# Performance work log

Measured on AMD Instinct MI355X. Metric: run time of the kernel, lower is better.

## Reference

```python
import jax, jax.numpy as jnp
import numpy as np

N, D_IN, D_HID, D_CODE, K = 131072, 768, 512, 256, 512

def setup_inputs() -> dict:
    key = jax.random.key(0)
    ks = jax.random.split(key, 10)
    s1 = 1.0 / np.sqrt(D_IN); s2 = 1.0 / np.sqrt(D_HID); s3 = 1.0 / np.sqrt(D_CODE)
    return {
        "x": jax.random.normal(ks[0], (N, D_IN), jnp.float32),
        "W1": jax.random.normal(ks[1], (D_IN, D_HID), jnp.float32) * s1,
        "b1": jnp.zeros((D_HID,), jnp.float32),
        "W2": jax.random.normal(ks[2], (D_HID, D_CODE), jnp.float32) * s2,
        "b2": jnp.zeros((D_CODE,), jnp.float32),
        "codebook": jax.random.normal(ks[3], (K, D_CODE), jnp.float32),
        "W3": jax.random.normal(ks[4], (D_CODE, D_HID), jnp.float32) * s3,
        "b3": jnp.zeros((D_HID,), jnp.float32),
        "W4": jax.random.normal(ks[5], (D_HID, D_IN), jnp.float32) * s2,
        "b4": jnp.zeros((D_IN,), jnp.float32),
    }

def reference(x, W1, b1, W2, b2, codebook, W3, b3, W4, b4):
    # encoder: Linear -> ReLU -> Linear
    z = jax.nn.relu(x @ W1 + b1) @ W2 + b2                      # [N, D_CODE]
    # nearest-code search: squared euclidean distances to codebook
    # ||z||^2 - 2 z.c + ||c||^2  (||z||^2 constant per row, drop for argmin)
    dots = z @ codebook.T                                        # [N, K]
    dist = jnp.sum(codebook * codebook, axis=-1)[None, :] - 2.0 * dots
    indices = jnp.argmin(dist, axis=-1)                          # [N] int
    quantized = codebook[indices]                                # gather [N, D_CODE]
    # commitment loss: mse(quantize.detach(), z) * commitment_weight(=1.0)
    commit_loss = jnp.mean((jax.lax.stop_gradient(quantized) - z) ** 2)
    # straight-through estimator
    quantized_st = z + jax.lax.stop_gradient(quantized - z)
    # decoder: Linear -> ReLU -> Linear
    recon = jax.nn.relu(quantized_st @ W3 + b3) @ W4 + b4        # [N, D_IN]
    return recon, indices.astype(jnp.int32), commit_loss
```

## Files before the change

### kernel.cpp

```cpp
#include <hip/hip_runtime.h>
#include <hip/hip_bf16.h>
#include <math.h>

#define N_ROWS 131072
#define DIN    768
#define DHID   512
#define DCODE  256
#define KC     512
#define NFUSE  768
#define TAU    5e-3f

typedef short short8 __attribute__((ext_vector_type(8)));
typedef float f32x4  __attribute__((ext_vector_type(4)));
typedef unsigned int   u32;
typedef unsigned short u16;

__device__ __forceinline__ void gload16(const void* g, void* l) {
    __builtin_amdgcn_global_load_lds(
        (const __attribute__((address_space(1))) u32*)g,
        (__attribute__((address_space(3))) u32*)l, 16, 0, 0);
}

__device__ __forceinline__ u16 f2bf(float f) {
    u32 u = __builtin_bit_cast(u32, f);
    return (u16)((u + 0x7fffu + ((u >> 16) & 1u)) >> 16);
}
__device__ __forceinline__ float bf2f(u16 h) {
    u32 u = ((u32)h) << 16;
    return __builtin_bit_cast(float, u);
}

__device__ __forceinline__ void xcd_swizzle(int& bxs, int& bys) {
    const int GX  = gridDim.x;
    const int nwg = GX * gridDim.y;
    const int lid = blockIdx.y * GX + blockIdx.x;
    const int chunk = nwg >> 3;
    const int nlid  = (lid & 7) * chunk + (lid >> 3);
    bxs = nlid % GX;
    bys = nlid / GX;
}

__device__ __forceinline__ void split_write(char* hidst, char* lodst, float4 v) {
    u16 h0 = f2bf(v.x), h1 = f2bf(v.y), h2 = f2bf(v.z), h3 = f2bf(v.w);
    u16 l0 = f2bf(__fsub_rn(v.x, bf2f(h0)));
    u16 l1 = f2bf(__fsub_rn(v.y, bf2f(h1)));
    u16 l2 = f2bf(__fsub_rn(v.z, bf2f(h2)));
    u16 l3 = f2bf(__fsub_rn(v.w, bf2f(h3)));
    ushort4 hi; hi.x = h0; hi.y = h1; hi.z = h2; hi.w = h3;
    ushort4 lo; lo.x = l0; lo.y = l1; lo.z = l2; lo.w = l3;
    *(ushort4*)hidst = hi;
    *(ushort4*)lodst = lo;
}

template<int EPI>
__global__ __launch_bounds__(256, 3)
void split2_gemm(const float* __restrict__ Af32,
                 const u16* __restrict__ Ahi, const u16* __restrict__ Alo,
                 const u16* __restrict__ Bhi, const u16* __restrict__ Blo,
                 const float* __restrict__ bias,
                 const float* __restrict__ cnorm,
                 u16* __restrict__ Chi, u16* __restrict__ Clo,
                 float* __restrict__ pd1, int* __restrict__ pi1,
                 float* __restrict__ pd2, float* __restrict__ pzn,
                 int M, int N, int K)
{
    __shared__ char lds[32768];
    const int t = threadIdx.x, lane = t & 63, wid = t >> 6;
    const int wm = wid >> 1, wn = wid & 1;
    int bxs, bys; xcd_swizzle(bxs, bys);
    const int bm = bys * 128, bn = bxs * 128;
    const bool full3 = (EPI == 0) || (bxs < 4);

    const int sr = lane >> 3, qq = lane & 7, sl = qq ^ sr;
    const u16* bsrc[4];
    #pragma unroll
    for (int c = 0; c < 4; c++) {
        int row = bn + (wid * 4 + c) * 8 + sr;
        const u16* base = (sl < 4) ? Bhi : Blo;
        bsrc[c] = base + (size_t)row * K + (sl & 3) * 8;
    }
    const u16* asrc[4];
    const float* a32src[4];
    int adhi[4], adlo[4];
    if constexpr (EPI == 1) {
        #pragma unroll
        for (int c = 0; c < 4; c++) {
            int row = bm + (wid * 4 + c) * 8 + sr;
            const u16* base = (sl < 4) ? Ahi : Alo;
            asrc[c] = base + (size_t)row * K + (sl & 3) * 8;
        }
    } else {
        #pragma unroll
        for (int c = 0; c < 4; c++) {
            int id = c * 256 + t;
            int row = id >> 3, k4 = id & 7;
            a32src[c] = Af32 + (size_t)(bm + row) * K + k4 * 4;
            int s = k4 >> 1, hf = k4 & 1;
            adhi[c] = row * 128 + ((s ^ (row & 7)) << 4) + hf * 8;
            adlo[c] = row * 128 + (((s | 4) ^ (row & 7)) << 4) + hf * 8;
        }
    }

    f32x4 acc[4][4];
    #pragma unroll
    for (int i = 0; i < 4; i++)
        #pragma unroll
        for (int j = 0; j < 4; j++) acc[i][j] = (f32x4)0.f;

    const int fr = lane & 15, sw = lane & 7;
    const int offhi = (((lane >> 4) ^ sw) << 4);
    const int offlo = ((((lane >> 4) | 4) ^ sw) << 4);
    const int arow = wm * 64 + fr, brow = wn * 64 + fr;
    const int NT = K >> 5;

    for (int tt = 0; tt < NT; tt++) {
        __syncthreads();
        const int kadv = tt * 32;
        #pragma unroll
        for (int c = 0; c < 4; c++)
            gload16(bsrc[c] + kadv, lds + 16384 + (wid * 4 + c) * 1024);
        if constexpr (EPI == 1) {
            #pragma unroll
            for (int c = 0; c < 4; c++)
                gload16(asrc[c] + kadv, lds + (wid * 4 + c) * 1024);
        } else {
            #pragma unroll
            for (int c = 0; c < 4; c++) {
                float4 v = *(const float4*)(a32src[c] + kadv);
                split_write(lds + adhi[c], lds + adlo[c], v);
            }
        }
        __syncthreads();
        char* ab  = lds;
        char* bb2 = lds + 16384;
        short8 ah[4], al[4];
        #pragma unroll
        for (int i = 0; i < 4; i++) {
            ah[i] = *(const short8*)(ab + ((arow + i * 16) << 7) + offhi);
            al[i] = *(const short8*)(ab + ((arow + i * 16) << 7) + offlo);
        }
        if (full3) {
            #pragma unroll
            for (int j = 0; j < 4; j++) {
                short8 bh = *(const short8*)(bb2 + ((brow + j * 16) << 7) + offhi);
                short8 bl = *(const short8*)(bb2 + ((brow + j * 16) << 7) + offlo);
                #pragma unroll
                for (int i = 0; i < 4; i++) {
                    acc[i][j] = __builtin_amdgcn_mfma_f32_16x16x32_bf16(ah[i], bh, acc[i][j], 0, 0, 0);
                    acc[i][j] = __builtin_amdgcn_mfma_f32_16x16x32_bf16(al[i], bh, acc[i][j], 0, 0, 0);
                    acc[i][j] = __builtin_amdgcn_mfma_f32_16x16x32_bf16(ah[i], bl, acc[i][j], 0, 0, 0);
                }
            }
        } else {
            #pragma unroll
            for (int j = 0; j < 4; j++) {
                short8 bh = *(const short8*)(bb2 + ((brow + j * 16) << 7) + offhi);
                #pragma unroll
                for (int i = 0; i < 4; i++)
                    acc[i][j] = __builtin_amdgcn_mfma_f32_16x16x32_bf16(ah[i], bh, acc[i][j], 0, 0, 0);
            }
        }
    }

    if constexpr (EPI == 1) {
        const int ec = lane & 15, g = lane >> 4;
        if (bxs < 4) {
            float cnv[4], bcv[4];
            #pragma unroll
            for (int j = 0; j < 4; j++) {
                int c = bn + wn * 64 + j * 16 + ec;
                cnv[j] = cnorm[c]; bcv[j] = bias[c];
            }
            const int strip = bxs * 2 + wn;
            #pragma unroll
            for (int i = 0; i < 4; i++) {
                #pragma unroll
                for (int e = 0; e < 4; e++) {
                    float d1 = INFINITY, d2 = INFINITY; int i1 = 0x7fffffff;
                    #pragma unroll
                    for (int j = 0; j < 4; j++) {
                        int c = bn + wn * 64 + j * 16 + ec;
                        float d = __fsub_rn(cnv[j],
                                  __fmul_rn(2.0f, __fadd_rn(acc[i][j][e], bcv[j])));
                        if (d < d1 || (d == d1 && c < i1)) { d2 = d1; d1 = d; i1 = c; }
                        else if (d < d2) d2 = d;
                    }
                    #pragma unroll
                    for (int m = 1; m < 16; m <<= 1) {
                        float od1 = __shfl_xor(d1, m);
                        int   oi1 = __shfl_xor(i1, m);
                        float od2 = __shfl_xor(d2, m);
                        if (od1 < d1 || (od1 == d1 && oi1 < i1)) {
                            d2 = fminf(d1, od2); d1 = od1; i1 = oi1;
                        } else d2 = fminf(d2, od1);
                    }
                    if (ec == 0) {
                        int r = bm + wm * 64 + i * 16 + g * 4 + e;
                        pd1[(size_t)strip * M + r] = d1;
                        pi1[(size_t)strip * M + r] = i1;
                        pd2[(size_t)strip * M + r] = d2;
                    }
                }
            }
        } else {
            float bcv[4];
            #pragma unroll
            for (int j = 0; j < 4; j++)
                bcv[j] = bias[bn + wn * 64 + j * 16 + ec];
            const int zs = (bxs - 4) * 2 + wn;
            #pragma unroll
            for (int i = 0; i < 4; i++) {
                #pragma unroll
                for (int e = 0; e < 4; e++) {
                    float s = 0.f;
                    #pragma unroll
                    for (int j = 0; j < 4; j++) {
                        float zv = acc[i][j][e] + bcv[j];
                        s = fmaf(zv, zv, s);
                    }
                    #pragma unroll
                    for (int m = 1; m < 16; m <<= 1) s += __shfl_xor(s, m);
                    if (ec == 0) {
                        int r = bm + wm * 64 + i * 16 + g * 4 + e;
                        pzn[(size_t)zs * M + r] = s;
                    }
                }
            }
        }
        return;
    } else {
        const int er = (lane >> 4) * 4, ec = lane & 15;
        #pragma unroll
        for (int j = 0; j < 4; j++) {
            int col = bn + wn * 64 + j * 16 + ec;
            float bb = bias[col];
            #pragma unroll
            for (int i = 0; i < 4; i++) {
                #pragma unroll
                for (int e = 0; e < 4; e++) {
                    int r = bm + wm * 64 + i * 16 + er + e;
                    float v = fmaxf(__fadd_rn(acc[i][j][e], bb), 0.f);
                    u16 hi = f2bf(v);
                    u16 lo = f2bf(__fsub_rn(v, bf2f(hi)));
                    Chi[(size_t)r * N + col] = hi;
                    Clo[(size_t)r * N + col] = lo;
                }
            }
        }
    }
}

template<bool RELU, bool OUT_BF16>
__global__ __launch_bounds__(256, 3)
void mfma_gemm(const u16* __restrict__ A, const u16* __restrict__ BT,
               const float* __restrict__ bias,
               void* __restrict__ Cout, int M, int N, int K)
{
    __shared__ char lds[32768];
    const int t    = threadIdx.x;
    const int lane = t & 63, wid = t >> 6;
    const int wm   = wid >> 1, wn = wid & 1;
    int bxs, bys;
    xcd_swizzle(bxs, bys);
    const int bm = bys * 128, bn = bxs * 128;

    const int sr = lane >> 3;
    const int sc = ((lane & 7) ^ sr) * 8;
    const u16* aptr[4];
    const u16* bptr[4];
    #pragma unroll
    for (int c = 0; c < 4; c++) {
        int gc   = wid * 4 + c;
        int arow = bm + 8 * gc + sr;
        aptr[c] = A  + (size_t)arow * K + sc;
        int brow = bn + 8 * gc + sr;
        bptr[c] = BT + (size_t)brow * K + sc;
    }

    f32x4 acc[4][4];
    #pragma unroll
    for (int i = 0; i < 4; i++)
        #pragma unroll
        for (int j = 0; j < 4; j++) acc[i][j] = (f32x4)0.f;

    const int koff0 = (16 * (lane >> 4))      ^ ((lane & 7) << 4);
    const int koff1 = (64 + 16 * (lane >> 4)) ^ ((lane & 7) << 4);
    const int arow_rd = wm * 64 + (lane & 15);
    const int brow_rd = wn * 64 + (lane & 15);

    const int NT = K >> 6;
    for (int tt = 0; tt < NT; tt++) {
        __syncthreads();
        const int k0 = tt << 6;
        #pragma unroll
        for (int c = 0; c < 4; c++) {
            int gc = wid * 4 + c;
            gload16(aptr[c] + k0, lds + gc * 1024);
            gload16(bptr[c] + k0, lds + 16384 + gc * 1024);
        }
        __syncthreads();
        char* ldsA = lds;
        char* ldsB = lds + 16384;
        #pragma unroll
        for (int kk = 0; kk < 2; kk++) {
            const int ko = kk ? koff1 : koff0;
            short8 af[4], bfr[4];
            #pragma unroll
            for (int i = 0; i < 4; i++)
                af[i]  = *(const short8*)(ldsA + (arow_rd + i * 16) * 128 + ko);
            #pragma unroll
            for (int j = 0; j < 4; j++)
                bfr[j] = *(const short8*)(ldsB + (brow_rd + j * 16) * 128 + ko);
            #pragma unroll
            for (int i = 0; i < 4; i++)
                #pragma unroll
                for (int j = 0; j < 4; j++)
                    acc[i][j] = __builtin_amdgcn_mfma_f32_16x16x32_bf16(
                        af[i], bfr[j], acc[i][j], 0, 0, 0);
        }
    }

    const int er = (lane >> 4) * 4;
    const int ec = lane & 15;
    #pragma unroll
    for (int j = 0; j < 4; j++) {
        int col  = bn + wn * 64 + j * 16 + ec;
        float bb = bias[col];
        #pragma unroll
        for (int i = 0; i < 4; i++) {
            #pragma unroll
            for (int e = 0; e < 4; e++) {
                int r   = bm + wm * 64 + i * 16 + er + e;
                float v = acc[i][j][e] + bb;
                if (RELU) v = fmaxf(v, 0.f);
                if (OUT_BF16) ((u16*)Cout)[(size_t)r * N + col]  = f2bf(v);
                else          ((float*)Cout)[(size_t)r * N + col] = v;
            }
        }
    }
}

__global__ __launch_bounds__(256)
void gather_out(const float* __restrict__ R, const int* __restrict__ idxi,
                float* __restrict__ out)
{
    int w    = (blockIdx.x * 256 + threadIdx.x) >> 6;
    int lane = threadIdx.x & 63;
    int nw   = (gridDim.x * 256) >> 6;
    for (int r = w; r < N_ROWS; r += nw) {
        int code = idxi[r];
        const float4* src = (const float4*)(R + (size_t)code * DIN);
        float4* dst = (float4*)(out + (size_t)r * DIN);
        dst[lane]       = src[lane];
        dst[lane + 64]  = src[lane + 64];
        dst[lane + 128] = src[lane + 128];
    }
}

__global__ void transpose_cb_kernel(const float* __restrict__ cb, float* __restrict__ cbT)
{
    int tid = blockIdx.x * 256 + threadIdx.x;
    int k = tid >> 8;
    int d = tid & 255;
    cbT[(size_t)d * KC + k] = cb[(size_t)k * DCODE + d];
}

__global__ void cast_bf16_kernel(const float* __restrict__ in, u16* __restrict__ out, int n)
{
    int i = blockIdx.x * 256 + threadIdx.x;
    if (i < n) out[i] = f2bf(in[i]);
}

__global__ void castT_bf16_kernel(const float* __restrict__ in, u16* __restrict__ out,
                                  int K, int N)
{
    int i = blockIdx.x * 256 + threadIdx.x;
    if (i >= K * N) return;
    int n = i / K, k = i - n * K;
    out[i] = f2bf(in[(size_t)k * N + n]);
}

__global__ void prep_W1T(const float* __restrict__ W1, u16* __restrict__ Thi,
                         u16* __restrict__ Tlo)
{
    int id = blockIdx.x * 256 + threadIdx.x;
    if (id >= DHID * DIN) return;
    int n = id / DIN, k = id - n * DIN;
    float v = W1[(size_t)k * DHID + n];
    u16 hi = f2bf(v);
    Thi[id] = hi;
    Tlo[id] = f2bf(__fsub_rn(v, bf2f(hi)));
}

__global__ void prep_Wc(const float* __restrict__ W2, const float* __restrict__ cb,
                        u16* __restrict__ Thi, u16* __restrict__ Tlo)
{
    int id = blockIdx.x * 256 + threadIdx.x;
    int n = id & 511, h = id >> 9;
    double acc = 0.0;
    for (int tt2 = 0; tt2 < DCODE; tt2++)
        acc += (double)W2[(size_t)h * DCODE + tt2] * (double)cb[(size_t)n * DCODE + tt2];
    float v = (float)acc;
    u16 hi = f2bf(v);
    Thi[(size_t)n * DHID + h] = hi;
    Tlo[(size_t)n * DHID + h] = f2bf(__fsub_rn(v, bf2f(hi)));
}

__global__ void prep_W2T_pair(const float* __restrict__ W2, u16* __restrict__ Thi,
                              u16* __restrict__ Tlo)
{
    int id = blockIdx.x * 256 + threadIdx.x;
    if (id >= DCODE * DHID) return;
    int t2 = id >> 9, h = id & 511;
    float v = W2[(size_t)h * DCODE + t2];
    u16 hi = f2bf(v);
    Thi[(size_t)(KC + t2) * DHID + h] = hi;
    Tlo[(size_t)(KC + t2) * DHID + h] = f2bf(__fsub_rn(v, bf2f(hi)));
}

__global__ void prep_bcf(const float* __restrict__ b2, const float* __restrict__ cb,
                         float* __restrict__ bcf)
{
    int n = blockIdx.x * 256 + threadIdx.x;
    if (n >= NFUSE) return;
    if (n < KC) {
        double acc = 0.0;
        for (int tt2 = 0; tt2 < DCODE; tt2++)
            acc += (double)b2[tt2] * (double)cb[(size_t)n * DCODE + tt2];
        bcf[n] = (float)acc;
    } else {
        bcf[n] = b2[n - KC];
    }
}

__global__ void cnorm_np_kernel(const float* __restrict__ cb, float* __restrict__ cnorm)
{
    int k = blockIdx.x * 64 + threadIdx.x;
    if (k >= KC) return;
    const float* c = cb + (size_t)k * DCODE;
    float bsum[2];
    #pragma unroll
    for (int b = 0; b < 2; b++) {
        const float* a = c + b * 128;
        float r[8];
        #pragma unroll
        for (int j = 0; j < 8; j++) r[j] = __fmul_rn(a[j], a[j]);
        for (int i = 8; i < 128; i += 8)
            #pragma unroll
            for (int j = 0; j < 8; j++)
                r[j] = __fadd_rn(r[j], __fmul_rn(a[i + j], a[i + j]));
        bsum[b] = __fadd_rn(
            __fadd_rn(__fadd_rn(r[0], r[1]), __fadd_rn(r[2], r[3])),
            __fadd_rn(__fadd_rn(r[4], r[5]), __fadd_rn(r[6], r[7])));
    }
    cnorm[k] = __fadd_rn(bsum[0], bsum[1]);
}

__global__ void final_argmin_flag(const float* __restrict__ pd1,
                                  const int* __restrict__ pi1,
                                  const float* __restrict__ pd2,
                                  const float* __restrict__ pzn,
                                  float* __restrict__ idx_f,
                                  int* __restrict__ idx_i,
                                  float* __restrict__ rowloss,
                                  int* __restrict__ cnt,
                                  int* __restrict__ list)
{
    int r = blockIdx.x * 256 + threadIdx.x;
    if (r >= N_ROWS) return;
    float d1 = pd1[r]; int i1 = pi1[r]; float d2 = pd2[r];
    #pragma unroll
    for (int b = 1; b < 8; b++) {
        float od1 = pd1[(size_t)b * N_ROWS + r];
        int   oi1 = pi1[(size_t)b * N_ROWS + r];
        float od2 = pd2[(size_t)b * N_ROWS + r];
        if (od1 < d1 || (od1 == d1 && oi1 < i1)) {
            d2 = fminf(d1, od2); d1 = od1; i1 = oi1;
        } else d2 = fminf(d2, od1);
    }
    float zn = pzn[r] + pzn[(size_t)N_ROWS + r]
             + pzn[(size_t)2 * N_ROWS + r] + pzn[(size_t)3 * N_ROWS + r];
    idx_f[r]   = (float)i1;
    idx_i[r]   = i1;
    rowloss[r] = zn + d1;
    if (d2 - d1 < TAU) {
        int p = atomicAdd(cnt, 1);
        list[p] = r;
    }
}

__global__ __launch_bounds__(512)
void recompute_kernel(const float* __restrict__ x,  const float* __restrict__ W1,
                      const float* __restrict__ b1, const float* __restrict__ W2,
                      const float* __restrict__ b2, const float* __restrict__ cbT,
                      const float* __restrict__ cnorm,
                      const int* __restrict__ cnt,  const int* __restrict__ list,
                      float* __restrict__ idx_f,    int* __restrict__ idx_i)
{
    __shared__ float xs[8][DIN];
    __shared__ float h1s[8][DHID];
    __shared__ float zs[8][DCODE];
    __shared__ float swd[8][8];
    __shared__ int   swi[8][8];
    __shared__ int   rls[8];
    const int t = threadIdx.x;
    const int n = *cnt;

    for (int base = blockIdx.x * 8; base < n; base += gridDim.x * 8) {
        __syncthreads();
        if (t < 8) rls[t] = (base + t < n) ? list[base + t] : -1;
        __syncthreads();
        #pragma unroll
        for (int rr = 0; rr < 8; rr++) {
            int row = rls[rr];
            if (row >= 0)
                for (int i = t; i < DIN; i += 512)
                    xs[rr][i] = x[(size_t)row * DIN + i];
        }
        __syncthreads();
        {
            float acc[8] = {0.f,0.f,0.f,0.f,0.f,0.f,0.f,0.f};
            for (int i = 0; i < DIN; i++) {
                float w = W1[(size_t)i * DHID + t];
                #pragma unroll
                for (int rr = 0; rr < 8; rr++)
                    acc[rr] = fmaf(xs[rr][i], w, acc[rr]);
            }
            float bb = b1[t];
            #pragma unroll
            for (int rr = 0; rr < 8; rr++)
                h1s[rr][t] = fmaxf(__fadd_rn(acc[rr], bb), 0.f);
        }
        __syncthreads();
        {
            int half = t >> 8, t2 = t & 255;
            float acc[4] = {0.f,0.f,0.f,0.f};
            for (int h = 0; h < DHID; h++) {
                float w = W2[(size_t)h * DCODE + t2];
                #pragma unroll
                for (int q2 = 0; q2 < 4; q2++)
                    acc[q2] = fmaf(h1s[half * 4 + q2][h], w, acc[q2]);
            }
            float bb = b2[t2];
            #pragma unroll
            for (int q2 = 0; q2 < 4; q2++)
                zs[half * 4 + q2][t2] = __fadd_rn(acc[q2], bb);
        }
        __syncthreads();
        {
            float acc[8] = {0.f,0.f,0.f,0.f,0.f,0.f,0.f,0.f};
            for (int d = 0; d < DCODE; d++) {
                float c = cbT[(size_t)d * KC + t];
                #pragma unroll
                for (int rr = 0; rr < 8; rr++)
                    acc[rr] = fmaf(zs[rr][d], c, acc[rr]);
            }
            float cn = cnorm[t];
            #pragma unroll
            for (int rr = 0; rr < 8; rr++) {
                float d = __fsub_rn(cn, __fmul_rn(2.0f, acc[rr]));
                int ii = t;
                #pragma unroll
                for (int m = 1; m < 64; m <<= 1) {
                    float od = __shfl_xor(d, m);
                    int   oi = __shfl_xor(ii, m);
                    if (od < d || (od == d && oi < ii)) { d = od; ii = oi; }
                }
                if ((t & 63) == 0) { swd[rr][t >> 6] = d; swi[rr][t >> 6] = ii; }
            }
        }
        __syncthreads();
        if (t < 8) {
            int row = rls[t];
            if (row >= 0) {
                float d = swd[t][0]; int ii = swi[t][0];
                #pragma unroll
                for (int w = 1; w < 8; w++) {
                    float od = swd[t][w]; int oi = swi[t][w];
                    if (od < d || (od == d && oi < ii)) { d = od; ii = oi; }
                }
                idx_i[row] = ii;
                idx_f[row] = (float)ii;
            }
        }
    }
}

__global__ void loss_reduce_kernel(const float* __restrict__ rowloss,
                                   double* __restrict__ acc, int n)
{
    double s = 0.0;
    for (int i = blockIdx.x * blockDim.x + threadIdx.x; i < n; i += gridDim.x * blockDim.x)
        s += (double)rowloss[i];
    for (int off = 32; off; off >>= 1) s += __shfl_xor(s, off);
    __shared__ double red[4];
    int lane = threadIdx.x & 63, wave = threadIdx.x >> 6;
    if (lane == 0) red[wave] = s;
    __syncthreads();
    if (threadIdx.x == 0) {
        double b = red[0] + red[1] + red[2] + red[3];
        atomicAdd(acc, b);
    }
}

__global__ void finalize_kernel(const double* __restrict__ acc, float* __restrict__ out)
{
    out[0] = (float)(acc[0] / ((double)N_ROWS * (double)DCODE));
}

extern "C" void kernel_launch(void* const* d_in, const int* in_sizes, int n_in,
                              void* d_out, int out_size, void* d_ws, size_t ws_size,
                              hipStream_t stream)
{
    const float* x  = (const float*)d_in[0];
    const float* W1 = (const float*)d_in[1];
    const float* b1 = (const float*)d_in[2];
    const float* W2 = (const float*)d_in[3];
    const float* b2 = (const float*)d_in[4];
    const float* cb = (const float*)d_in[5];
    const float* W3 = (const float*)d_in[6];
    const float* b3 = (const float*)d_in[7];
    const float* W4 = (const float*)d_in[8];
    const float* b4 = (const float*)d_in[9];
    float* out = (float*)d_out;
    char*  ws  = (char*)d_ws;

    u16*    h1hi    = (u16*)   (ws);
    u16*    h1lo    = (u16*)   (ws + 134217728);
    float*  pd1     = (float*) (ws + 268435456);
    int*    pi1     = (int*)   (ws + 272629760);
    float*  pd2     = (float*) (ws + 276824064);
    float*  pzn     = (float*) (ws + 281018368);
    float*  rowloss = (float*) (ws + 283115520);
    int*    idxi    = (int*)   (ws + 283639808);
    int*    list    = (int*)   (ws + 284164096);
    int*    rcnt    = (int*)   (ws + 284688384);
    double* lossa   = (double*)(ws + 284688448);
    u16*    W1Thi   = (u16*)   (ws + 284688512);
    u16*    W1Tlo   = (u16*)   (ws + 285474944);
    u16*    WfThi   = (u16*)   (ws + 286261376);
    u16*    WfTlo   = (u16*)   (ws + 287047808);
    u16*    cbB     = (u16*)   (ws + 287834240);
    u16*    W3T     = (u16*)   (ws + 288096384);
    u16*    W4T     = (u16*)   (ws + 288358528);
    float*  bcf     = (float*) (ws + 289144960);
    float*  cnorm   = (float*) (ws + 289148032);
    float*  cbT     = (float*) (ws + 289150080);
    u16*    R1b     = (u16*)   (ws + 289674368);
    float*  Rf      = (float*) (ws + 290198656);

    float* idxf    = out + (size_t)N_ROWS * DIN;
    float* lossout = idxf + N_ROWS;

    hipMemsetAsync(ws + 284688384, 0, 128, stream);

    transpose_cb_kernel<<<512, 256, 0, stream>>>(cb, cbT);
    cnorm_np_kernel<<<8, 64, 0, stream>>>(cb, cnorm);
    cast_bf16_kernel<<<(KC*DCODE)/256, 256, 0, stream>>>(cb, cbB, KC*DCODE);
    castT_bf16_kernel<<<(DCODE*DHID)/256, 256, 0, stream>>>(W3, W3T, DCODE, DHID);
    castT_bf16_kernel<<<(DHID*DIN)/256, 256, 0, stream>>>(W4, W4T, DHID, DIN);
    prep_W1T<<<(DHID*DIN)/256, 256, 0, stream>>>(W1, W1Thi, W1Tlo);
    prep_Wc<<<(KC*DHID)/256, 256, 0, stream>>>(W2, cb, WfThi, WfTlo);
    prep_W2T_pair<<<(DCODE*DHID)/256, 256, 0, stream>>>(W2, WfThi, WfTlo);
    prep_bcf<<<3, 256, 0, stream>>>(b2, cb, bcf);

    mfma_gemm<true,  true ><<<dim3(4, 4), 256, 0, stream>>>(
        cbB, W3T, b3, (void*)R1b, KC, DHID, DCODE);
    mfma_gemm<false, false><<<dim3(6, 4), 256, 0, stream>>>(
        R1b, W4T, b4, (void*)Rf, KC, DIN, DHID);

    split2_gemm<0><<<dim3(DHID/128, N_ROWS/128), 256, 0, stream>>>(
        x, nullptr, nullptr, W1Thi, W1Tlo, b1, nullptr,
        h1hi, h1lo, nullptr, nullptr, nullptr, nullptr, N_ROWS, DHID, DIN);
    split2_gemm<1><<<dim3(NFUSE/128, N_ROWS/128), 256, 0, stream>>>(
        nullptr, h1hi, h1lo, WfThi, WfTlo, bcf, cnorm,
        nullptr, nullptr, pd1, pi1, pd2, pzn, N_ROWS, NFUSE, DHID);

    final_argmin_flag<<<N_ROWS/256, 256, 0, stream>>>(
        pd1, pi1, pd2, pzn, idxf, idxi, rowloss, rcnt, list);
    recompute_kernel<<<2048, 512, 0, stream>>>(
        x, W1, b1, W2, b2, cbT, cnorm, rcnt, list, idxf, idxi);

    gather_out<<<4096, 256, 0, stream>>>(Rf, idxi, out);

    loss_reduce_kernel<<<256, 256, 0, stream>>>(rowloss, lossa, N_ROWS);
    finalize_kernel<<<1, 1, 0, stream>>>(lossa, lossout);
}
```

Baseline: 942.0 us.

## Drop split-bf16 emulation; use plain bf16 GEMMs with wider recompute margin

Replaces the three-MFMA hi/lo split-bf16 emulation of fp32 in the encoder and distance GEMMs with single-pass bf16 GEMMs. The hidden activations are stored only as bf16, and the K-step grows from 32 to 64. This removes about two thirds of the MFMA work and half of the h1 traffic. To compensate for lower precision, the near-tie threshold TAU is raised from 5e-3 to 1.5, so many more rows fall into the exact fp32 recompute path, which could become costly.

```diff
diff --git a/kernel.cpp b/kernel.cpp
--- a/kernel.cpp
+++ b/kernel.cpp
@@ -8,7 +8,7 @@
 #define DCODE  256
 #define KC     512
 #define NFUSE  768
-#define TAU    5e-3f
+#define TAU    1.5f
 
 typedef short short8 __attribute__((ext_vector_type(8)));
 typedef float f32x4  __attribute__((ext_vector_type(4)));
@@ -40,210 +40,230 @@
     bys = nlid / GX;
 }
 
-__device__ __forceinline__ void split_write(char* hidst, char* lodst, float4 v) {
-    u16 h0 = f2bf(v.x), h1 = f2bf(v.y), h2 = f2bf(v.z), h3 = f2bf(v.w);
-    u16 l0 = f2bf(__fsub_rn(v.x, bf2f(h0)));
-    u16 l1 = f2bf(__fsub_rn(v.y, bf2f(h1)));
-    u16 l2 = f2bf(__fsub_rn(v.z, bf2f(h2)));
-    u16 l3 = f2bf(__fsub_rn(v.w, bf2f(h3)));
-    ushort4 hi; hi.x = h0; hi.y = h1; hi.z = h2; hi.w = h3;
-    ushort4 lo; lo.x = l0; lo.y = l1; lo.z = l2; lo.w = l3;
-    *(ushort4*)hidst = hi;
-    *(ushort4*)lodst = lo;
-}
-
-template<int EPI>
 __global__ __launch_bounds__(256, 3)
-void split2_gemm(const float* __restrict__ Af32,
-                 const u16* __restrict__ Ahi, const u16* __restrict__ Alo,
-                 const u16* __restrict__ Bhi, const u16* __restrict__ Blo,
-                 const float* __restrict__ bias,
-                 const float* __restrict__ cnorm,
-                 u16* __restrict__ Chi, u16* __restrict__ Clo,
-                 float* __restrict__ pd1, int* __restrict__ pi1,
-                 float* __restrict__ pd2, float* __restrict__ pzn,
-                 int M, int N, int K)
+void h1_gemm(const float* __restrict__ x, const u16* __restrict__ W1T,
+             const float* __restrict__ b1, u16* __restrict__ h1b,
+             int M, int N, int K)
 {
     __shared__ char lds[32768];
     const int t = threadIdx.x, lane = t & 63, wid = t >> 6;
     const int wm = wid >> 1, wn = wid & 1;
     int bxs, bys; xcd_swizzle(bxs, bys);
     const int bm = bys * 128, bn = bxs * 128;
-    const bool full3 = (EPI == 0) || (bxs < 4);
-
-    const int sr = lane >> 3, qq = lane & 7, sl = qq ^ sr;
-    const u16* bsrc[4];
+
+    const int sr = lane >> 3;
+    const int sc = ((lane & 7) ^ sr) * 8;
+    const u16* bptr[4];
     #pragma unroll
     for (int c = 0; c < 4; c++) {
-        int row = bn + (wid * 4 + c) * 8 + sr;
-        const u16* base = (sl < 4) ? Bhi : Blo;
-        bsrc[c] = base + (size_t)row * K + (sl & 3) * 8;
-    }
-    const u16* asrc[4];
-    const float* a32src[4];
-    int adhi[4], adlo[4];
-    if constexpr (EPI == 1) {
+        int brow = bn + 8 * (wid * 4 + c) + sr;
+        bptr[c] = W1T + (size_t)brow * K + sc;
+    }
+    const float* asrc[4];
+    int albyte[4];
+    #pragma unroll
+    for (int c = 0; c < 4; c++) {
+        int id = c * 256 + t;
+        int row = id >> 3, g = id & 7;
+        asrc[c]   = x + (size_t)(bm + row) * K + g * 8;
+        albyte[c] = row * 128 + ((g ^ (row & 7)) << 4);
+    }
+
+    f32x4 acc[4][4];
+    #pragma unroll
+    for (int i = 0; i < 4; i++)
+        #pragma unroll
+        for (int j = 0; j < 4; j++) acc[i][j] = (f32x4)0.f;
+
+    const int koff0 = (16 * (lane >> 4))      ^ ((lane & 7) << 4);
+    const int koff1 = (64 + 16 * (lane >> 4)) ^ ((lane & 7) << 4);
+    const int arow_rd = wm * 64 + (lane & 15);
+    const int brow_rd = wn * 64 + (lane & 15);
+
+    const int NT = K >> 6;
+    for (int tt = 0; tt < NT; tt++) {
+        __syncthreads();
+        const int k0 = tt << 6;
+        #pragma unroll
+        for (int c = 0; c < 4; c++)
+            gload16(bptr[c] + k0, lds + 16384 + (wid * 4 + c) * 1024);
         #pragma unroll
         for (int c = 0; c < 4; c++) {
-            int row = bm + (wid * 4 + c) * 8 + sr;
-            const u16* base = (sl < 4) ? Ahi : Alo;
-            asrc[c] = base + (size_t)row * K + (sl & 3) * 8;
+            float4 v0 = *(const float4*)(asrc[c] + k0);
+            float4 v1 = *(const float4*)(asrc[c] + k0 + 4);
+            short8 p;
+            p[0] = (short)f2bf(v0.x); p[1] = (short)f2bf(v0.y);
+            p[2] = (short)f2bf(v0.z); p[3] = (short)f2bf(v0.w);
+            p[4] = (short)f2bf(v1.x); p[5] = (short)f2bf(v1.y);
+            p[6] = (short)f2bf(v1.z); p[7] = (short)f2bf(v1.w);
+            *(short8*)(lds + albyte[c]) = p;
+        }
+        __syncthreads();
+        char* ldsA = lds;
+        char* ldsB = lds + 16384;
+        #pragma unroll
+        for (int kk = 0; kk < 2; kk++) {
+            const int ko = kk ? koff1 : koff0;
+            short8 af[4], bfr[4];
+            #pragma unroll
+            for (int i = 0; i < 4; i++)
+                af[i]  = *(const short8*)(ldsA + (arow_rd + i * 16) * 128 + ko);
+            #pragma unroll
+            for (int j = 0; j < 4; j++)
+                bfr[j] = *(const short8*)(ldsB + (brow_rd + j * 16) * 128 + ko);
+            #pragma unroll
+            for (int i = 0; i < 4; i++)
+                #pragma unroll
+                for (int j = 0; j < 4; j++)
+                    acc[i][j] = __builtin_amdgcn_mfma_f32_16x16x32_bf16(
+                        af[i], bfr[j], acc[i][j], 0, 0, 0);
+        }
+    }
+
+    const int er = (lane >> 4) * 4, ec = lane & 15;
+    #pragma unroll
+    for (int j = 0; j < 4; j++) {
+        int col  = bn + wn * 64 + j * 16 + ec;
+        float bb = b1[col];
+        #pragma unroll
+        for (int i = 0; i < 4; i++) {
+            #pragma unroll
+            for (int e = 0; e < 4; e++) {
+                int r   = bm + wm * 64 + i * 16 + er + e;
+                float v = fmaxf(acc[i][j][e] + bb, 0.f);
+                h1b[(size_t)r * N + col] = f2bf(v);
+            }
+        }
+    }
+}
+
+__global__ __launch_bounds__(256, 3)
+void dots_gemm(const u16* __restrict__ A, const u16* __restrict__ BT,
+               const float* __restrict__ bias, const float* __restrict__ cnorm,
+               float* __restrict__ pd1, int* __restrict__ pi1,
+               float* __restrict__ pd2, float* __restrict__ pzn,
+               int M, int N, int K)
+{
+    __shared__ char lds[32768];
+    const int t = threadIdx.x, lane = t & 63, wid = t >> 6;
+    const int wm = wid >> 1, wn = wid & 1;
+    int bxs, bys; xcd_swizzle(bxs, bys);
+    const int bm = bys * 128, bn = bxs * 128;
+
+    const int sr = lane >> 3;
+    const int sc = ((lane & 7) ^ sr) * 8;
+    const u16* aptr[4];
+    const u16* bptr[4];
+    #pragma unroll
+    for (int c = 0; c < 4; c++) {
+        int gc = wid * 4 + c;
+        aptr[c] = A  + (size_t)(bm + 8 * gc + sr) * K + sc;
+        bptr[c] = BT + (size_t)(bn + 8 * gc + sr) * K + sc;
+    }
+
+    f32x4 acc[4][4];
+    #pragma unroll
+    for (int i = 0; i < 4; i++)
+        #pragma unroll
+        for (int j = 0; j < 4; j++) acc[i][j] = (f32x4)0.f;
+
+    const int koff0 = (16 * (lane >> 4))      ^ ((lane & 7) << 4);
+    const int koff1 = (64 + 16 * (lane >> 4)) ^ ((lane & 7) << 4);
+    const int arow_rd = wm * 64 + (lane & 15);
+    const int brow_rd = wn * 64 + (lane & 15);
+
+    const int NT = K >> 6;
+    for (int tt = 0; tt < NT; tt++) {
+        __syncthreads();
+        const int k0 = tt << 6;
+        #pragma unroll
+        for (int c = 0; c < 4; c++) {
+            int gc = wid * 4 + c;
+            gload16(aptr[c] + k0, lds + gc * 1024);
+            gload16(bptr[c] + k0, lds + 16384 + gc * 1024);
+        }
+        __syncthreads();
+        char* ldsA = lds;
+        char* ldsB = lds + 16384;
+        #pragma unroll
+        for (int kk = 0; kk < 2; kk++) {
+            const int ko = kk ? koff1 : koff0;
+            short8 af[4], bfr[4];
+            #pragma unroll
+            for (int i = 0; i < 4; i++)
+                af[i]  = *(const short8*)(ldsA + (arow_rd + i * 16) * 128 + ko);
+            #pragma unroll
+            for (int j = 0; j < 4; j++)
+                bfr[j] = *(const short8*)(ldsB + (brow_rd + j * 16) * 128 + ko);
+            #pragma unroll
+            for (int i = 0; i < 4; i++)
+                #pragma unroll
+                for (int j = 0; j < 4; j++)
+                    acc[i][j] = __builtin_amdgcn_mfma_f32_16x16x32_bf16(
+                        af[i], bfr[j], acc[i][j], 0, 0, 0);
+        }
+    }
+
+    const int ec = lane & 15, g = lane >> 4;
+    if (bxs < 4) {
+        float cnv[4], bcv[4];
+        #pragma unroll
+        for (int j = 0; j < 4; j++) {
+            int c = bn + wn * 64 + j * 16 + ec;
+            cnv[j] = cnorm[c]; bcv[j] = bias[c];
+        }
+        const int strip = bxs * 2 + wn;
+        #pragma unroll
+        for (int i = 0; i < 4; i++) {
+            #pragma unroll
+            for (int e = 0; e < 4; e++) {
+                float d1 = INFINITY, d2 = INFINITY; int i1 = 0x7fffffff;
+                #pragma unroll
+                for (int j = 0; j < 4; j++) {
+                    int c = bn + wn * 64 + j * 16 + ec;
+                    float d = __fsub_rn(cnv[j],
+                              __fmul_rn(2.0f, __fadd_rn(acc[i][j][e], bcv[j])));
+                    if (d < d1 || (d == d1 && c < i1)) { d2 = d1; d1 = d; i1 = c; }
+                    else if (d < d2) d2 = d;
+                }
+                #pragma unroll
+                for (int m = 1; m < 16; m <<= 1) {
+                    float od1 = __shfl_xor(d1, m);
+                    int   oi1 = __shfl_xor(i1, m);
+                    float od2 = __shfl_xor(d2, m);
+                    if (od1 < d1 || (od1 == d1 && oi1 < i1)) {
+                        d2 = fminf(d1, od2); d1 = od1; i1 = oi1;
+                    } else d2 = fminf(d2, od1);
+                }
+                if (ec == 0) {
+                    int r = bm + wm * 64 + i * 16 + g * 4 + e;
+                    pd1[(size_t)strip * M + r] = d1;
+                    pi1[(size_t)strip * M + r] = i1;
+                    pd2[(size_t)strip * M + r] = d2;
+                }
+            }
         }
     } else {
-        #pragma unroll
-        for (int c = 0; c < 4; c++) {
-            int id = c * 256 + t;
-            int row = id >> 3, k4 = id & 7;
-            a32src[c] = Af32 + (size_t)(bm + row) * K + k4 * 4;
-            int s = k4 >> 1, hf = k4 & 1;
-            adhi[c] = row * 128 + ((s ^ (row & 7)) << 4) + hf * 8;
-            adlo[c] = row * 128 + (((s | 4) ^ (row & 7)) << 4) + hf * 8;
-        }
-    }
-
-    f32x4 acc[4][4];
-    #pragma unroll
-    for (int i = 0; i < 4; i++)
-        #pragma unroll
-        for (int j = 0; j < 4; j++) acc[i][j] = (f32x4)0.f;
-
-    const int fr = lane & 15, sw = lane & 7;
-    const int offhi = (((lane >> 4) ^ sw) << 4);
-    const int offlo = ((((lane >> 4) | 4) ^ sw) << 4);
-    const int arow = wm * 64 + fr, brow = wn * 64 + fr;
-    const int NT = K >> 5;
-
-    for (int tt = 0; tt < NT; tt++) {
-        __syncthreads();
-        const int kadv = tt * 32;
-        #pragma unroll
-        for (int c = 0; c < 4; c++)
-            gload16(bsrc[c] + kadv, lds + 16384 + (wid * 4 + c) * 1024);
-        if constexpr (EPI == 1) {
-            #pragma unroll
-            for (int c = 0; c < 4; c++)
-                gload16(asrc[c] + kadv, lds + (wid * 4 + c) * 1024);
-        } else {
-            #pragma unroll
-            for (int c = 0; c < 4; c++) {
-                float4 v = *(const float4*)(a32src[c] + kadv);
-                split_write(lds + adhi[c], lds + adlo[c], v);
-            }
-        }
-        __syncthreads();
-        char* ab  = lds;
-        char* bb2 = lds + 16384;
-        short8 ah[4], al[4];
+        float bcv[4];
+        #pragma unroll
+        for (int j = 0; j < 4; j++)
+            bcv[j] = bias[bn + wn * 64 + j * 16 + ec];
+        const int zs = (bxs - 4) * 2 + wn;
         #pragma unroll
         for (int i = 0; i < 4; i++) {
-            ah[i] = *(const short8*)(ab + ((arow + i * 16) << 7) + offhi);
-            al[i] = *(const short8*)(ab + ((arow + i * 16) << 7) + offlo);
-        }
-        if (full3) {
-            #pragma unroll
-            for (int j = 0; j < 4; j++) {
-                short8 bh = *(const short8*)(bb2 + ((brow + j * 16) << 7) + offhi);
-                short8 bl = *(const short8*)(bb2 + ((brow + j * 16) << 7) + offlo);
-                #pragma unroll
-                for (int i = 0; i < 4; i++) {
-                    acc[i][j] = __builtin_amdgcn_mfma_f32_16x16x32_bf16(ah[i], bh, acc[i][j], 0, 0, 0);
-                    acc[i][j] = __builtin_amdgcn_mfma_f32_16x16x32_bf16(al[i], bh, acc[i][j], 0, 0, 0);
-                    acc[i][j] = __builtin_amdgcn_mfma_f32_16x16x32_bf16(ah[i], bl, acc[i][j], 0, 0, 0);
+            #pragma unroll
+            for (int e = 0; e < 4; e++) {
+                float s = 0.f;
+                #pragma unroll
+                for (int j = 0; j < 4; j++) {
+                    float zv = acc[i][j][e] + bcv[j];
+                    s = fmaf(zv, zv, s);
                 }
-            }
-        } else {
-            #pragma unroll
-            for (int j = 0; j < 4; j++) {
-                short8 bh = *(const short8*)(bb2 + ((brow + j * 16) << 7) + offhi);
-                #pragma unroll
-                for (int i = 0; i < 4; i++)
-                    acc[i][j] = __builtin_amdgcn_mfma_f32_16x16x32_bf16(ah[i], bh, acc[i][j], 0, 0, 0);
-            }
-        }
-    }
-
-    if constexpr (EPI == 1) {
-        const int ec = lane & 15, g = lane >> 4;
-        if (bxs < 4) {
-            float cnv[4], bcv[4];
-            #pragma unroll
-            for (int j = 0; j < 4; j++) {
-                int c = bn + wn * 64 + j * 16 + ec;
-                cnv[j] = cnorm[c]; bcv[j] = bias[c];
-            }
-            const int strip = bxs * 2 + wn;
-            #pragma unroll
-            for (int i = 0; i < 4; i++) {
-                #pragma unroll
-                for (int e = 0; e < 4; e++) {
-                    float d1 = INFINITY, d2 = INFINITY; int i1 = 0x7fffffff;
-                    #pragma unroll
-                    for (int j = 0; j < 4; j++) {
-                        int c = bn + wn * 64 + j * 16 + ec;
-                        float d = __fsub_rn(cnv[j],
-                                  __fmul_rn(2.0f, __fadd_rn(acc[i][j][e], bcv[j])));
-                        if (d < d1 || (d == d1 && c < i1)) { d2 = d1; d1 = d; i1 = c; }
-                        else if (d < d2) d2 = d;
-                    }
-                    #pragma unroll
-                    for (int m = 1; m < 16; m <<= 1) {
-                        float od1 = __shfl_xor(d1, m);
-                        int   oi1 = __shfl_xor(i1, m);
-                        float od2 = __shfl_xor(d2, m);
-                        if (od1 < d1 || (od1 == d1 && oi1 < i1)) {
-                            d2 = fminf(d1, od2); d1 = od1; i1 = oi1;
-                        } else d2 = fminf(d2, od1);
-                    }
-                    if (ec == 0) {
-                        int r = bm + wm * 64 + i * 16 + g * 4 + e;
-                        pd1[(size_t)strip * M + r] = d1;
-                        pi1[(size_t)strip * M + r] = i1;
-                        pd2[(size_t)strip * M + r] = d2;
-                    }
-                }
-            }
-        } else {
-            float bcv[4];
-            #pragma unroll
-            for (int j = 0; j < 4; j++)
-                bcv[j] = bias[bn + wn * 64 + j * 16 + ec];
-            const int zs = (bxs - 4) * 2 + wn;
-            #pragma unroll
-            for (int i = 0; i < 4; i++) {
-                #pragma unroll
-                for (int e = 0; e < 4; e++) {
-                    float s = 0.f;
-                    #pragma unroll
-                    for (int j = 0; j < 4; j++) {
-                        float zv = acc[i][j][e] + bcv[j];
-                        s = fmaf(zv, zv, s);
-                    }
-                    #pragma unroll
-                    for (int m = 1; m < 16; m <<= 1) s += __shfl_xor(s, m);
-                    if (ec == 0) {
-                        int r = bm + wm * 64 + i * 16 + g * 4 + e;
-                        pzn[(size_t)zs * M + r] = s;
-                    }
-                }
-            }
-        }
-        return;
-    } else {
-        const int er = (lane >> 4) * 4, ec = lane & 15;
-        #pragma unroll
-        for (int j = 0; j < 4; j++) {
-            int col = bn + wn * 64 + j * 16 + ec;
-            float bb = bias[col];
-            #pragma unroll
-            for (int i = 0; i < 4; i++) {
-                #pragma unroll
-                for (int e = 0; e < 4; e++) {
-                    int r = bm + wm * 64 + i * 16 + er + e;
-                    float v = fmaxf(__fadd_rn(acc[i][j][e], bb), 0.f);
-                    u16 hi = f2bf(v);
-                    u16 lo = f2bf(__fsub_rn(v, bf2f(hi)));
-                    Chi[(size_t)r * N + col] = hi;
-                    Clo[(size_t)r * N + col] = lo;
+                #pragma unroll
+                for (int m = 1; m < 16; m <<= 1) s += __shfl_xor(s, m);
+                if (ec == 0) {
+                    int r = bm + wm * 64 + i * 16 + g * 4 + e;
+                    pzn[(size_t)zs * M + r] = s;
                 }
             }
         }
@@ -271,10 +291,8 @@
     #pragma unroll
     for (int c = 0; c < 4; c++) {
         int gc   = wid * 4 + c;
-        int arow = bm + 8 * gc + sr;
-        aptr[c] = A  + (size_t)arow * K + sc;
-        int brow = bn + 8 * gc + sr;
-        bptr[c] = BT + (size_t)brow * K + sc;
+        aptr[c] = A  + (size_t)(bm + 8 * gc + sr) * K + sc;
+        bptr[c] = BT + (size_t)(bn + 8 * gc + sr) * K + sc;
     }
 
     f32x4 acc[4][4];
@@ -380,42 +398,23 @@
     out[i] = f2bf(in[(size_t)k * N + n]);
 }
 
-__global__ void prep_W1T(const float* __restrict__ W1, u16* __restrict__ Thi,
-                         u16* __restrict__ Tlo)
-{
-    int id = blockIdx.x * 256 + threadIdx.x;
-    if (id >= DHID * DIN) return;
-    int n = id / DIN, k = id - n * DIN;
-    float v = W1[(size_t)k * DHID + n];
-    u16 hi = f2bf(v);
-    Thi[id] = hi;
-    Tlo[id] = f2bf(__fsub_rn(v, bf2f(hi)));
-}
-
 __global__ void prep_Wc(const float* __restrict__ W2, const float* __restrict__ cb,
-                        u16* __restrict__ Thi, u16* __restrict__ Tlo)
+                        u16* __restrict__ T)
 {
     int id = blockIdx.x * 256 + threadIdx.x;
     int n = id & 511, h = id >> 9;
     double acc = 0.0;
     for (int tt2 = 0; tt2 < DCODE; tt2++)
         acc += (double)W2[(size_t)h * DCODE + tt2] * (double)cb[(size_t)n * DCODE + tt2];
-    float v = (float)acc;
-    u16 hi = f2bf(v);
-    Thi[(size_t)n * DHID + h] = hi;
-    Tlo[(size_t)n * DHID + h] = f2bf(__fsub_rn(v, bf2f(hi)));
-}
-
-__global__ void prep_W2T_pair(const float* __restrict__ W2, u16* __restrict__ Thi,
-                              u16* __restrict__ Tlo)
+    T[(size_t)n * DHID + h] = f2bf((float)acc);
+}
+
+__global__ void prep_W2T(const float* __restrict__ W2, u16* __restrict__ T)
 {
     int id = blockIdx.x * 256 + threadIdx.x;
     if (id >= DCODE * DHID) return;
     int t2 = id >> 9, h = id & 511;
-    float v = W2[(size_t)h * DCODE + t2];
-    u16 hi = f2bf(v);
-    Thi[(size_t)(KC + t2) * DHID + h] = hi;
-    Tlo[(size_t)(KC + t2) * DHID + h] = f2bf(__fsub_rn(v, bf2f(hi)));
+    T[(size_t)(KC + t2) * DHID + h] = f2bf(W2[(size_t)h * DCODE + t2]);
 }
 
 __global__ void prep_bcf(const float* __restrict__ b2, const float* __restrict__ cb,
@@ -625,43 +624,40 @@
     float* out = (float*)d_out;
     char*  ws  = (char*)d_ws;
 
-    u16*    h1hi    = (u16*)   (ws);
-    u16*    h1lo    = (u16*)   (ws + 134217728);
-    float*  pd1     = (float*) (ws + 268435456);
-    int*    pi1     = (int*)   (ws + 272629760);
-    float*  pd2     = (float*) (ws + 276824064);
-    float*  pzn     = (float*) (ws + 281018368);
-    float*  rowloss = (float*) (ws + 283115520);
-    int*    idxi    = (int*)   (ws + 283639808);
-    int*    list    = (int*)   (ws + 284164096);
-    int*    rcnt    = (int*)   (ws + 284688384);
-    double* lossa   = (double*)(ws + 284688448);
-    u16*    W1Thi   = (u16*)   (ws + 284688512);
-    u16*    W1Tlo   = (u16*)   (ws + 285474944);
-    u16*    WfThi   = (u16*)   (ws + 286261376);
-    u16*    WfTlo   = (u16*)   (ws + 287047808);
-    u16*    cbB     = (u16*)   (ws + 287834240);
-    u16*    W3T     = (u16*)   (ws + 288096384);
-    u16*    W4T     = (u16*)   (ws + 288358528);
-    float*  bcf     = (float*) (ws + 289144960);
-    float*  cnorm   = (float*) (ws + 289148032);
-    float*  cbT     = (float*) (ws + 289150080);
-    u16*    R1b     = (u16*)   (ws + 289674368);
-    float*  Rf      = (float*) (ws + 290198656);
+    u16*    h1b     = (u16*)   (ws);
+    float*  pd1     = (float*) (ws + 134217728);
+    int*    pi1     = (int*)   (ws + 138412032);
+    float*  pd2     = (float*) (ws + 142606336);
+    float*  pzn     = (float*) (ws + 146800640);
+    float*  rowloss = (float*) (ws + 148897792);
+    int*    idxi    = (int*)   (ws + 149422080);
+    int*    list    = (int*)   (ws + 149946368);
+    int*    rcnt    = (int*)   (ws + 150470656);
+    double* lossa   = (double*)(ws + 150470720);
+    u16*    W1Tb    = (u16*)   (ws + 150470784);
+    u16*    Wfb     = (u16*)   (ws + 151257216);
+    u16*    cbB     = (u16*)   (ws + 152043648);
+    u16*    W3T     = (u16*)   (ws + 152305792);
+    u16*    W4T     = (u16*)   (ws + 152567936);
+    float*  bcf     = (float*) (ws + 153354368);
+    float*  cnorm   = (float*) (ws + 153357440);
+    float*  cbT     = (float*) (ws + 153359488);
+    u16*    R1b     = (u16*)   (ws + 153883776);
+    float*  Rf      = (float*) (ws + 154408064);
 
     float* idxf    = out + (size_t)N_ROWS * DIN;
     float* lossout = idxf + N_ROWS;
 
-    hipMemsetAsync(ws + 284688384, 0, 128, stream);
+    hipMemsetAsync(ws + 150470656, 0, 128, stream);
 
     transpose_cb_kernel<<<512, 256, 0, stream>>>(cb, cbT);
     cnorm_np_kernel<<<8, 64, 0, stream>>>(cb, cnorm);
     cast_bf16_kernel<<<(KC*DCODE)/256, 256, 0, stream>>>(cb, cbB, KC*DCODE);
     castT_bf16_kernel<<<(DCODE*DHID)/256, 256, 0, stream>>>(W3, W3T, DCODE, DHID);
     castT_bf16_kernel<<<(DHID*DIN)/256, 256, 0, stream>>>(W4, W4T, DHID, DIN);
-    prep_W1T<<<(DHID*DIN)/256, 256, 0, stream>>>(W1, W1Thi, W1Tlo);
-    prep_Wc<<<(KC*DHID)/256, 256, 0, stream>>>(W2, cb, WfThi, WfTlo);
-    prep_W2T_pair<<<(DCODE*DHID)/256, 256, 0, stream>>>(W2, WfThi, WfTlo);
+    castT_bf16_kernel<<<(DIN*DHID)/256, 256, 0, stream>>>(W1, W1Tb, DIN, DHID);
+    prep_Wc<<<(KC*DHID)/256, 256, 0, stream>>>(W2, cb, Wfb);
+    prep_W2T<<<(DCODE*DHID)/256, 256, 0, stream>>>(W2, Wfb);
     prep_bcf<<<3, 256, 0, stream>>>(b2, cb, bcf);
 
     mfma_gemm<true,  true ><<<dim3(4, 4), 256, 0, stream>>>(
@@ -669,12 +665,10 @@
     mfma_gemm<false, false><<<dim3(6, 4), 256, 0, stream>>>(
         R1b, W4T, b4, (void*)Rf, KC, DIN, DHID);
 
-    split2_gemm<0><<<dim3(DHID/128, N_ROWS/128), 256, 0, stream>>>(
-        x, nullptr, nullptr, W1Thi, W1Tlo, b1, nullptr,
-        h1hi, h1lo, nullptr, nullptr, nullptr, nullptr, N_ROWS, DHID, DIN);
-    split2_gemm<1><<<dim3(NFUSE/128, N_ROWS/128), 256, 0, stream>>>(
-        nullptr, h1hi, h1lo, WfThi, WfTlo, bcf, cnorm,
-        nullptr, nullptr, pd1, pi1, pd2, pzn, N_ROWS, NFUSE, DHID);
+    h1_gemm<<<dim3(DHID/128, N_ROWS/128), 256, 0, stream>>>(
+        x, W1Tb, b1, h1b, N_ROWS, DHID, DIN);
+    dots_gemm<<<dim3(NFUSE/128, N_ROWS/128), 256, 0, stream>>>(
+        h1b, Wfb, bcf, cnorm, pd1, pi1, pd2, pzn, N_ROWS, NFUSE, DHID);
 
     final_argmin_flag<<<N_ROWS/256, 256, 0, stream>>>(
         pd1, pi1, pd2, pzn, idxf, idxi, rowloss, rcnt, list);
```

Measured after the change: 1.368 ms. 1.45x slower.
